# Kernel optimization log

Measured on AMD Instinct MI355X. Metric: run time of the kernel, lower is better.

The kernel has to match this reference:

```python
import jax, jax.numpy as jnp
import numpy as np

B, S, D, H = 4, 4096, 256, 4
Dh = D // H


def setup_inputs() -> dict:
    key = jax.random.key(0)
    ks = jax.random.split(key, 5)
    scale = 1.0 / np.sqrt(D)
    return {
        "inputs": jax.random.normal(ks[0], (B, S, D), dtype=jnp.float32),
        "Wq": jax.random.normal(ks[1], (D, D), dtype=jnp.float32) * scale,
        "bq": jnp.zeros((D,), jnp.float32),
        "Wk": jax.random.normal(ks[2], (D, D), dtype=jnp.float32) * scale,
        "bk": jnp.zeros((D,), jnp.float32),
        "Wv": jax.random.normal(ks[3], (D, D), dtype=jnp.float32) * scale,
        "bv": jnp.zeros((D,), jnp.float32),
        "Wo": jax.random.normal(ks[4], (D, D), dtype=jnp.float32) * scale,
        "bo": jnp.zeros((D,), jnp.float32),
    }


def reference(inputs, Wq, bq, Wk, bk, Wv, bv, Wo, bo):
    b, s, d = inputs.shape
    # QKV projections
    q = inputs @ Wq + bq
    k = inputs @ Wk + bk
    v = inputs @ Wv + bv
    # separate heads: [B, S, D] -> [B, H, S, Dh]
    def split_heads(x):
        return x.reshape(b, s, H, Dh).transpose(0, 2, 1, 3)
    q, k, v = split_heads(q), split_heads(k), split_heads(v)
    # scaled dot-product attention (no causal mask: mask=False)
    scores = jnp.einsum("bhqd,bhkd->bhqk", q, k) / jnp.sqrt(jnp.float32(Dh))
    weights = jax.nn.softmax(scores, axis=-1)
    attn = jnp.einsum("bhqk,bhkd->bhqd", weights, v)
    # combine heads: [B, H, S, Dh] -> [B, S, D]
    attn = attn.transpose(0, 2, 1, 3).reshape(b, s, d)
    return attn @ Wo + bo
```

## Files before the change

kernel.cpp:

```cpp
#include <hip/hip_runtime.h>
#include <cmath>

#define B_  4
#define S_  4096
#define D_  256
#define H_  4
#define DH_ 64
#define M_TOTAL (B_*S_)
#define QSCALE 0.1803368801111f

typedef __bf16 bf16x8 __attribute__((ext_vector_type(8)));
typedef __bf16 bf16x4 __attribute__((ext_vector_type(4)));
typedef __bf16 bf16x2 __attribute__((ext_vector_type(2)));
typedef float  f32x4  __attribute__((ext_vector_type(4)));
typedef float  f32x16 __attribute__((ext_vector_type(16)));

#define AS1 __attribute__((address_space(1)))
#define AS3 __attribute__((address_space(3)))

__device__ __forceinline__ void g2lds16(const void* g, void* l) {
    __builtin_amdgcn_global_load_lds((AS1 const void*)g, (AS3 void*)l, 16, 0, 0);
}

#if __has_builtin(__builtin_amdgcn_permlane32_swap)
typedef unsigned uint2v __attribute__((ext_vector_type(2)));
__device__ __forceinline__ void plswap(unsigned &a, unsigned &b) {
    uint2v r = __builtin_amdgcn_permlane32_swap(a, b, false, false);
    a = r[0]; b = r[1];
}
#else
__device__ __forceinline__ void plswap(unsigned &a, unsigned &b) {
    unsigned bl = (unsigned)__shfl_xor((int)b, 32);
    unsigned ah = (unsigned)__shfl_xor((int)a, 32);
    bool hi = (threadIdx.x & 32) != 0;
    unsigned na = hi ? bl : a;
    unsigned nb = hi ? b  : ah;
    a = na; b = nb;
}
#endif

__device__ __forceinline__ unsigned pk2(float x, float y) {
    bf16x2 t; t[0] = (__bf16)x; t[1] = (__bf16)y;
    return __builtin_bit_cast(unsigned, t);
}

__global__ __launch_bounds__(256) void prep(const float* __restrict__ X,
                                            const float* __restrict__ W0,
                                            const float* __restrict__ W1,
                                            const float* __restrict__ W2,
                                            const float* __restrict__ W3,
                                            __bf16* __restrict__ Xb,
                                            __bf16* __restrict__ Wt_all) {
    int t = threadIdx.x;
    if (blockIdx.x < 2048) {
        size_t i = ((size_t)blockIdx.x * 256 + t) * 8;
        float4 v0 = *(const float4*)(X + i);
        float4 v1 = *(const float4*)(X + i + 4);
        bf16x8 o;
        o[0] = (__bf16)v0.x; o[1] = (__bf16)v0.y; o[2] = (__bf16)v0.z; o[3] = (__bf16)v0.w;
        o[4] = (__bf16)v1.x; o[5] = (__bf16)v1.y; o[6] = (__bf16)v1.z; o[7] = (__bf16)v1.w;
        *(bf16x8*)(Xb + i) = o;
        return;
    }
    int bid = blockIdx.x - 2048;
    int z = bid >> 6, rem = bid & 63;
    int by = rem >> 3, bx = rem & 7;
    const float* W = (z == 0) ? W0 : (z == 1) ? W1 : (z == 2) ? W2 : W3;
    float wsc = (z == 0) ? QSCALE : 1.0f;
    __bf16* Wt = Wt_all + (size_t)z * 65536;
    __shared__ float tile[32][33];
    int r0 = by * 32, c0 = bx * 32;
#pragma unroll
    for (int e = 0; e < 4; e++) {
        int idx = t + e * 256; int r = idx >> 5, c = idx & 31;
        tile[r][c] = W[(r0 + r) * 256 + c0 + c];
    }
    __syncthreads();
#pragma unroll
    for (int e = 0; e < 4; e++) {
        int idx = t + e * 256; int r = idx >> 5, c = idx & 31;
        Wt[(c0 + r) * 256 + (r0 + c)] = (__bf16)(tile[c][r] * wsc);
    }
}

__global__ __launch_bounds__(256, 3) void gemm_bt(const __bf16* __restrict__ A,
                                                  const __bf16* __restrict__ Wt_all,
                                                  const float* __restrict__ bias0,
                                                  const float* __restrict__ bias1,
                                                  const float* __restrict__ bias2,
                                                  __bf16* __restrict__ outb,
                                                  __bf16* __restrict__ voutb,
                                                  float* __restrict__ outf,
                                                  int out_is_f32, float bsc0) {
    constexpr int K = 256;
    __shared__ __attribute__((aligned(16))) __bf16 As[3 * 4096];
    __shared__ __attribute__((aligned(16))) __bf16 Bs[3 * 4096];

    int t = threadIdx.x;
    int lane = t & 63, w = t >> 6;
    int wr = w >> 1, wc = w & 1;
    int l16 = lane & 15, quad = lane >> 4;
    int mbase = blockIdx.x * 128;
    int nbase = blockIdx.y * 128;
    int z = blockIdx.z;
    const __bf16* Bt = Wt_all + (size_t)z * 65536;
    const float* bias = (z == 0) ? bias0 : (z == 1) ? bias1 : bias2;
    float bscale = (z == 0) ? bsc0 : 1.0f;

    f32x4 acc[4][4] = {};

    int srow = t >> 2;
    int sseg = (t & 3) * 8;

#define GSTAGE(kk, slot) do {                                                  \
        g2lds16(A  + (size_t)(mbase +      srow) * K + (kk) + sseg,            \
                (char*)As + (slot) * 8192 +        t * 16);                    \
        g2lds16(A  + (size_t)(mbase + 64 + srow) * K + (kk) + sseg,            \
                (char*)As + (slot) * 8192 + 4096 + t * 16);                    \
        g2lds16(Bt + (size_t)(nbase +      srow) * K + (kk) + sseg,            \
                (char*)Bs + (slot) * 8192 +        t * 16);                    \
        g2lds16(Bt + (size_t)(nbase + 64 + srow) * K + (kk) + sseg,            \
                (char*)Bs + (slot) * 8192 + 4096 + t * 16);                    \
    } while (0)

    GSTAGE(0, 0);
    GSTAGE(32, 1);

    int rs = 0, ps = 2;
#pragma unroll 1
    for (int s = 0; s < 8; s++) {
        if (s < 7) asm volatile("s_waitcnt vmcnt(4)" ::: "memory");
        else       asm volatile("s_waitcnt vmcnt(0)" ::: "memory");
        asm volatile("s_barrier" ::: "memory");
        if (s < 6) GSTAGE((s + 2) * 32, ps);

        bf16x8 a[4], b[4];
#pragma unroll
        for (int i = 0; i < 4; i++)
            a[i] = *(const bf16x8*)(As + rs * 4096 + (wr * 64 + i * 16 + l16) * 32 + quad * 8);
#pragma unroll
        for (int j = 0; j < 4; j++)
            b[j] = *(const bf16x8*)(Bs + rs * 4096 + (wc * 64 + j * 16 + l16) * 32 + quad * 8);
#pragma unroll
        for (int i = 0; i < 4; i++)
#pragma unroll
            for (int j = 0; j < 4; j++)
                acc[i][j] = __builtin_amdgcn_mfma_f32_16x16x32_bf16(a[i], b[j], acc[i][j], 0, 0, 0);

        rs = (rs == 2) ? 0 : rs + 1;
        ps = (ps == 2) ? 0 : ps + 1;
    }
#undef GSTAGE

#pragma unroll
    for (int i = 0; i < 4; i++) {
#pragma unroll
        for (int j = 0; j < 4; j++) {
            int col = nbase + wc * 64 + j * 16 + l16;
            float bv = bias[col] * bscale;
            int row0 = mbase + wr * 64 + i * 16 + quad * 4;
            if (out_is_f32) {
#pragma unroll
                for (int r = 0; r < 4; r++)
                    outf[(size_t)(row0 + r) * 256 + col] = acc[i][j][r] + bv;
            } else if (z == 2) {
                int hcol = col >> 6, dh = col & 63;
                int bidx = row0 >> 12, s0 = row0 & 4095;
                bf16x4 pk;
#pragma unroll
                for (int r = 0; r < 4; r++) pk[r] = (__bf16)(acc[i][j][r] + bv);
                *(bf16x4*)(voutb + ((size_t)(bidx * 4 + hcol) * 64 + dh) * 4096 + s0) = pk;
            } else {
#pragma unroll
                for (int r = 0; r < 4; r++)
                    outb[(size_t)z * ((size_t)M_TOTAL * 256) + (size_t)(row0 + r) * 256 + col] =
                        (__bf16)(acc[i][j][r] + bv);
            }
        }
    }
}

__global__ __launch_bounds__(256, 2) void attn(const __bf16* __restrict__ Qb,
                                               const __bf16* __restrict__ Kb,
                                               const __bf16* __restrict__ Vt,
                                               __bf16* __restrict__ Ctx) {
    __shared__ __attribute__((aligned(16))) __bf16 smem[32768];

    int t = threadIdx.x;
    int lane = t & 63, w = t >> 6;
    int l31 = lane & 31, hh = lane >> 5;
    int kw = w & 1, qw2 = w >> 1;

    int lin = blockIdx.x;
    int xcd = lin & 7, j = lin >> 3;
    int bh = xcd * 2 + (j & 1);
    int qblk = j >> 1;
    int b = bh >> 2, hd = bh & 3;
    int qw = qblk * 128 + qw2 * 64;

    const __bf16* Kbase = Kb + (size_t)b * S_ * 256 + hd * 64;
    const __bf16* Vbase = Vt + (size_t)bh * 64 * S_;

    bf16x8 qf[4][2];
#pragma unroll
    for (int ks = 0; ks < 4; ks++)
#pragma unroll
        for (int qt = 0; qt < 2; qt++)
            qf[ks][qt] = *(const bf16x8*)(Qb + (size_t)(b * S_ + qw + qt * 32 + l31) * 256
                                              + hd * 64 + ks * 16 + hh * 8);

    f32x16 acc[2][2] = {};
    float lsum[2] = {0.f, 0.f};

    int srow = t >> 3;
    int sseg = t & 7;

#define STAGE(kv, slot) do {                                                   \
        char* mk = (char*)smem + (slot) * 16384;                               \
        char* mv = mk + 8192;                                                  \
        _Pragma("unroll")                                                      \
        for (int c = 0; c < 2; c++) {                                          \
            int rr = c * 32 + srow;                                            \
            int gseg = (sseg ^ (rr & 7)) * 8;                                  \
            g2lds16(Kbase + (size_t)((kv) + rr) * 256 + gseg,                  \
                    mk + c * 4096 + t * 16);                                   \
            g2lds16(Vbase + (size_t)rr * S_ + (kv) + gseg,                     \
                    mv + c * 4096 + t * 16);                                   \
        }                                                                      \
    } while (0)

#define QKSTEP(TILE, SN) do {                                                  \
        __bf16* Ksp = (__bf16*)((char*)smem + ((TILE) & 3) * 16384);           \
        bf16x8 kfv[4];                                                         \
        _Pragma("unroll")                                                      \
        for (int ks = 0; ks < 4; ks++) {                                       \
            int slot = (ks * 2 + hh) ^ (l31 & 7);                              \
            kfv[ks] = *(const bf16x8*)(Ksp + (kw * 32 + l31) * 64 + slot * 8); \
        }                                                                      \
        _Pragma("unroll")                                                      \
        for (int qt = 0; qt < 2; qt++) SN[qt] = (f32x16){};                    \
        _Pragma("unroll")                                                      \
        for (int ks = 0; ks < 4; ks++)                                         \
            _Pragma("unroll")                                                  \
            for (int qt = 0; qt < 2; qt++)                                     \
                SN[qt] = __builtin_amdgcn_mfma_f32_32x32x16_bf16(              \
                    kfv[ks], qf[ks][qt], SN[qt], 0, 0, 0);                     \
    } while (0)

#define SMPV(IT, SC) do {                                                      \
        __bf16* Vsp = (__bf16*)((char*)smem + ((IT) & 3) * 16384) + 4096;      \
        unsigned dd[2][8];                                                     \
        _Pragma("unroll")                                                      \
        for (int qt = 0; qt < 2; qt++) {                                       \
            float p[16];                                                       \
            _Pragma("unroll")                                                  \
            for (int r = 0; r < 16; r++)                                       \
                p[r] = __builtin_amdgcn_exp2f(SC[qt][r]);                      \
            float s0 = ((p[0]+p[1])+(p[2]+p[3]))+((p[4]+p[5])+(p[6]+p[7]));    \
            float s1 = ((p[8]+p[9])+(p[10]+p[11]))+((p[12]+p[13])+(p[14]+p[15])); \
            lsum[qt] += s0 + s1;                                               \
            _Pragma("unroll")                                                  \
            for (int m = 0; m < 4; m++) {                                      \
                dd[qt][m*2]   = pk2(p[4*m],   p[4*m+1]);                       \
                dd[qt][m*2+1] = pk2(p[4*m+2], p[4*m+3]);                       \
            }                                                                  \
        }                                                                      \
        _Pragma("unroll")                                                      \
        for (int tt = 0; tt < 2; tt++) {                                       \
            int tks = kw * 2 + tt;                                             \
            bf16x8 pf[2];                                                      \
            _Pragma("unroll")                                                  \
            for (int qt = 0; qt < 2; qt++) {                                   \
                unsigned x0 = dd[qt][4*tt],   y0 = dd[qt][4*tt+2];             \
                unsigned x1 = dd[qt][4*tt+1], y1 = dd[qt][4*tt+3];             \
                plswap(x0, y0);                                                \
                plswap(x1, y1);                                                \
                union { unsigned u[4]; bf16x8 v; } c;                          \
                c.u[0] = x0; c.u[1] = x1; c.u[2] = y0; c.u[3] = y1;            \
                pf[qt] = c.v;                                                  \
            }                                                                  \
            _Pragma("unroll")                                                  \
            for (int mt = 0; mt < 2; mt++) {                                   \
                int slot = (tks * 2 + hh) ^ (l31 & 7);                         \
                bf16x8 vf = *(const bf16x8*)(Vsp + (mt*32 + l31)*64 + slot*8); \
                _Pragma("unroll")                                              \
                for (int qt = 0; qt < 2; qt++)                                 \
                    acc[mt][qt] = __builtin_amdgcn_mfma_f32_32x32x16_bf16(     \
                        vf, pf[qt], acc[mt][qt], 0, 0, 0);                     \
            }                                                                  \
        }                                                                      \
    } while (0)

#define BODY(IT, SC, SN) do {                                                  \
        if ((IT) < 62) asm volatile("s_waitcnt vmcnt(4)" ::: "memory");        \
        else           asm volatile("s_waitcnt vmcnt(0)" ::: "memory");        \
        asm volatile("s_barrier" ::: "memory");                                \
        if ((IT) <= 60) STAGE(((IT) + 3) * 64, ((IT) + 3) & 3);                \
        if ((IT) < 63) QKSTEP((IT) + 1, SN);                                   \
        SMPV(IT, SC);                                                          \
    } while (0)

    f32x16 stA[2], stB[2];

    STAGE(0, 0);
    STAGE(64, 1);
    STAGE(128, 2);
    asm volatile("s_waitcnt vmcnt(8)" ::: "memory");
    asm volatile("s_barrier" ::: "memory");
    QKSTEP(0, stA);

    for (int it = 0; it < 64; it += 2) {
        BODY(it,     stA, stB);
        BODY(it + 1, stB, stA);
    }
#undef BODY
#undef SMPV
#undef QKSTEP
#undef STAGE

#pragma unroll
    for (int qt = 0; qt < 2; qt++)
        lsum[qt] += __shfl_xor(lsum[qt], 32);

    __syncthreads();
    float* lsd = (float*)((char*)smem + 32768);
    if (kw == 1) {
#pragma unroll
        for (int mt = 0; mt < 2; mt++)
#pragma unroll
            for (int qt = 0; qt < 2; qt++)
#pragma unroll
                for (int g = 0; g < 4; g++) {
                    f32x4 v;
#pragma unroll
                    for (int e = 0; e < 4; e++) v[e] = acc[mt][qt][4 * g + e];
                    *(f32x4*)((char*)smem + qw2 * 16384
                              + ((mt * 2 + qt) * 4 + g) * 1024 + lane * 16) = v;
                }
        lsd[qw2 * 128 + lane * 2 + 0] = lsum[0];
        lsd[qw2 * 128 + lane * 2 + 1] = lsum[1];
    }
    __syncthreads();
    if (kw == 0) {
        float inv[2];
#pragma unroll
        for (int qt = 0; qt < 2; qt++)
            inv[qt] = 1.f / (lsum[qt] + lsd[qw2 * 128 + lane * 2 + qt]);
#pragma unroll
        for (int mt = 0; mt < 2; mt++)
#pragma unroll
            for (int qt = 0; qt < 2; qt++)
#pragma unroll
                for (int g = 0; g < 4; g++) {
                    f32x4 v = *(const f32x4*)((char*)smem + qw2 * 16384
                                              + ((mt * 2 + qt) * 4 + g) * 1024 + lane * 16);
#pragma unroll
                    for (int e = 0; e < 4; e++) acc[mt][qt][4 * g + e] += v[e];
                }

        __bf16* Es = smem + 18432 + qw2 * 4608;
#pragma unroll
        for (int qt = 0; qt < 2; qt++)
#pragma unroll
            for (int mt = 0; mt < 2; mt++)
#pragma unroll
                for (int rg = 0; rg < 4; rg++) {
                    bf16x4 ov;
#pragma unroll
                    for (int e = 0; e < 4; e++)
                        ov[e] = (__bf16)(acc[mt][qt][4 * rg + e] * inv[qt]);
                    int dhb = mt * 32 + rg * 8 + 4 * hh;
                    *(bf16x4*)(Es + (qt * 32 + l31) * 72 + dhb) = ov;
                }
#pragma unroll
        for (int pass = 0; pass < 8; pass++) {
            int q = pass * 8 + (lane >> 3);
            int col = (lane & 7) * 8;
            bf16x8 val = *(const bf16x8*)(Es + q * 72 + col);
            *(bf16x8*)(Ctx + (size_t)(b * S_ + qw + q) * 256 + hd * 64 + col) = val;
        }
    }
}

extern "C" void kernel_launch(void* const* d_in, const int* in_sizes, int n_in,
                              void* d_out, int out_size, void* d_ws, size_t ws_size,
                              hipStream_t stream) {
    const float* X  = (const float*)d_in[0];
    const float* Wq = (const float*)d_in[1];
    const float* bq = (const float*)d_in[2];
    const float* Wk = (const float*)d_in[3];
    const float* bk = (const float*)d_in[4];
    const float* Wv = (const float*)d_in[5];
    const float* bv = (const float*)d_in[6];
    const float* Wo = (const float*)d_in[7];
    const float* bo = (const float*)d_in[8];
    float* out = (float*)d_out;

    char* ws = (char*)d_ws;
    const size_t MB = 1024 * 1024;
    __bf16* Xb  = (__bf16*)(ws);
    __bf16* Ctx = (__bf16*)(ws);
    __bf16* Wt  = (__bf16*)(ws + 8 * MB);
    __bf16* Qb  = (__bf16*)(ws + 8 * MB + 512 * 1024);
    __bf16* Kb  = (__bf16*)((char*)Qb + 8 * MB);
    __bf16* Vt  = (__bf16*)((char*)Kb + 8 * MB);

    prep<<<dim3(2304), dim3(256), 0, stream>>>(X, Wq, Wk, Wv, Wo, Xb, Wt);
    gemm_bt<<<dim3(M_TOTAL / 128, 2, 3), dim3(256), 0, stream>>>(
        Xb, Wt, bq, bk, bv, Qb, Vt, nullptr, 0, QSCALE);
    attn<<<dim3(512), dim3(256), 0, stream>>>(Qb, Kb, Vt, Ctx);
    gemm_bt<<<dim3(M_TOTAL / 128, 2, 1), dim3(256), 0, stream>>>(
        Ctx, Wt + 3 * 65536, bo, bo, bo, nullptr, nullptr, out, 1, 1.0f);
}
```

Baseline: 180.6 us.

## Remap GEMM blocks to XCDs for L2 reuse and peel attention loop tail

The GEMM grid becomes a linear 1D launch. Each block's index is decoded so that blocks sharing an M tile (across the N halves and the Q/K/V weights) land on the same XCD, which should let the activation tile be reused from that XCD's L2. The attention main loop is restructured into a steady-state body unrolled by four with no conditional waits or staging, followed by an explicitly peeled tail of four iterations. This removes per-iteration branch logic, at the cost of larger code and more hand-maintained schedule correctness.

```diff
diff --git a/kernel.cpp b/kernel.cpp
--- a/kernel.cpp
+++ b/kernel.cpp
@@ -100,9 +100,19 @@
     int lane = t & 63, w = t >> 6;
     int wr = w >> 1, wc = w & 1;
     int l16 = lane & 15, quad = lane >> 4;
-    int mbase = blockIdx.x * 128;
-    int nbase = blockIdx.y * 128;
-    int z = blockIdx.z;
+
+    int lin = blockIdx.x;
+    int xcd = lin & 7, i = lin >> 3;
+    int mb, nb, z;
+    if (out_is_f32) {
+        mb = i >> 1; nb = i & 1; z = 0;
+    } else {
+        int nz = i % 6; mb = i / 6;
+        z = nz % 3; nb = nz / 3;
+    }
+    int mbase = (mb * 8 + xcd) * 128;
+    int nbase = nb * 128;
+
     const __bf16* Bt = Wt_all + (size_t)z * 65536;
     const float* bias = (z == 0) ? bias0 : (z == 1) ? bias1 : bias2;
     float bscale = (z == 0) ? bsc0 : 1.0f;
@@ -136,16 +146,16 @@
 
         bf16x8 a[4], b[4];
 #pragma unroll
-        for (int i = 0; i < 4; i++)
-            a[i] = *(const bf16x8*)(As + rs * 4096 + (wr * 64 + i * 16 + l16) * 32 + quad * 8);
+        for (int i2 = 0; i2 < 4; i2++)
+            a[i2] = *(const bf16x8*)(As + rs * 4096 + (wr * 64 + i2 * 16 + l16) * 32 + quad * 8);
 #pragma unroll
         for (int j = 0; j < 4; j++)
             b[j] = *(const bf16x8*)(Bs + rs * 4096 + (wc * 64 + j * 16 + l16) * 32 + quad * 8);
 #pragma unroll
-        for (int i = 0; i < 4; i++)
+        for (int i2 = 0; i2 < 4; i2++)
 #pragma unroll
             for (int j = 0; j < 4; j++)
-                acc[i][j] = __builtin_amdgcn_mfma_f32_16x16x32_bf16(a[i], b[j], acc[i][j], 0, 0, 0);
+                acc[i2][j] = __builtin_amdgcn_mfma_f32_16x16x32_bf16(a[i2], b[j], acc[i2][j], 0, 0, 0);
 
         rs = (rs == 2) ? 0 : rs + 1;
         ps = (ps == 2) ? 0 : ps + 1;
@@ -153,28 +163,28 @@
 #undef GSTAGE
 
 #pragma unroll
-    for (int i = 0; i < 4; i++) {
+    for (int i2 = 0; i2 < 4; i2++) {
 #pragma unroll
         for (int j = 0; j < 4; j++) {
             int col = nbase + wc * 64 + j * 16 + l16;
             float bv = bias[col] * bscale;
-            int row0 = mbase + wr * 64 + i * 16 + quad * 4;
+            int row0 = mbase + wr * 64 + i2 * 16 + quad * 4;
             if (out_is_f32) {
 #pragma unroll
                 for (int r = 0; r < 4; r++)
-                    outf[(size_t)(row0 + r) * 256 + col] = acc[i][j][r] + bv;
+                    outf[(size_t)(row0 + r) * 256 + col] = acc[i2][j][r] + bv;
             } else if (z == 2) {
                 int hcol = col >> 6, dh = col & 63;
                 int bidx = row0 >> 12, s0 = row0 & 4095;
                 bf16x4 pk;
 #pragma unroll
-                for (int r = 0; r < 4; r++) pk[r] = (__bf16)(acc[i][j][r] + bv);
+                for (int r = 0; r < 4; r++) pk[r] = (__bf16)(acc[i2][j][r] + bv);
                 *(bf16x4*)(voutb + ((size_t)(bidx * 4 + hcol) * 64 + dh) * 4096 + s0) = pk;
             } else {
 #pragma unroll
                 for (int r = 0; r < 4; r++)
                     outb[(size_t)z * ((size_t)M_TOTAL * 256) + (size_t)(row0 + r) * 256 + col] =
-                        (__bf16)(acc[i][j][r] + bv);
+                        (__bf16)(acc[i2][j][r] + bv);
             }
         }
     }
@@ -291,12 +301,11 @@
         }                                                                      \
     } while (0)
 
-#define BODY(IT, SC, SN) do {                                                  \
-        if ((IT) < 62) asm volatile("s_waitcnt vmcnt(4)" ::: "memory");        \
-        else           asm volatile("s_waitcnt vmcnt(0)" ::: "memory");        \
+#define BODYF(IT, SC, SN) do {                                                 \
+        asm volatile("s_waitcnt vmcnt(4)" ::: "memory");                       \
         asm volatile("s_barrier" ::: "memory");                                \
-        if ((IT) <= 60) STAGE(((IT) + 3) * 64, ((IT) + 3) & 3);                \
-        if ((IT) < 63) QKSTEP((IT) + 1, SN);                                   \
+        STAGE(((IT) + 3) * 64, ((IT) + 3) & 3);                                \
+        QKSTEP((IT) + 1, SN);                                                  \
         SMPV(IT, SC);                                                          \
     } while (0)
 
@@ -309,11 +318,32 @@
     asm volatile("s_barrier" ::: "memory");
     QKSTEP(0, stA);
 
-    for (int it = 0; it < 64; it += 2) {
-        BODY(it,     stA, stB);
-        BODY(it + 1, stB, stA);
-    }
-#undef BODY
+#pragma unroll 1
+    for (int i4 = 0; i4 < 15; i4++) {
+        int it = i4 * 4;
+        BODYF(it,     stA, stB);
+        BODYF(it + 1, stB, stA);
+        BODYF(it + 2, stA, stB);
+        BODYF(it + 3, stB, stA);
+    }
+
+    asm volatile("s_waitcnt vmcnt(4)" ::: "memory");
+    asm volatile("s_barrier" ::: "memory");
+    STAGE(63 * 64, 3);
+    QKSTEP(61, stB);
+    SMPV(60, stA);
+    asm volatile("s_waitcnt vmcnt(4)" ::: "memory");
+    asm volatile("s_barrier" ::: "memory");
+    QKSTEP(62, stA);
+    SMPV(61, stB);
+    asm volatile("s_waitcnt vmcnt(0)" ::: "memory");
+    asm volatile("s_barrier" ::: "memory");
+    QKSTEP(63, stB);
+    SMPV(62, stA);
+    asm volatile("s_waitcnt vmcnt(0)" ::: "memory");
+    asm volatile("s_barrier" ::: "memory");
+    SMPV(63, stB);
+#undef BODYF
 #undef SMPV
 #undef QKSTEP
 #undef STAGE
@@ -406,9 +436,9 @@
     __bf16* Vt  = (__bf16*)((char*)Kb + 8 * MB);
 
     prep<<<dim3(2304), dim3(256), 0, stream>>>(X, Wq, Wk, Wv, Wo, Xb, Wt);
-    gemm_bt<<<dim3(M_TOTAL / 128, 2, 3), dim3(256), 0, stream>>>(
+    gemm_bt<<<dim3(768), dim3(256), 0, stream>>>(
         Xb, Wt, bq, bk, bv, Qb, Vt, nullptr, 0, QSCALE);
     attn<<<dim3(512), dim3(256), 0, stream>>>(Qb, Kb, Vt, Ctx);
-    gemm_bt<<<dim3(M_TOTAL / 128, 2, 1), dim3(256), 0, stream>>>(
+    gemm_bt<<<dim3(256), dim3(256), 0, stream>>>(
         Ctx, Wt + 3 * 65536, bo, bo, bo, nullptr, nullptr, out, 1, 1.0f);
 }
```

After: 178.7 us. About the same (-1.0%).
